# Kernel optimization log

Hardware: AMD Instinct MI355X
Metric: run time of the kernel (lower is better)

## Reference

```python
import jax, jax.numpy as jnp
import numpy as np
from jax import lax

H, W = 480, 640
EPS = 1e-20
DN = ('NCHW', 'OIHW', 'NCHW')


def _nconv(x, c, w_raw, b, pad):
    # Normalized convolution: positive weights via softplus (EnforcePos hook).
    w = jax.nn.softplus(w_raw)                     # (O, I, kh, kw)
    pads = [(pad, pad), (pad, pad)]
    denom = lax.conv_general_dilated(c, w, (1, 1), pads, dimension_numbers=DN)
    nomin = lax.conv_general_dilated(x * c, w, (1, 1), pads, dimension_numbers=DN)
    out = nomin / (denom + EPS) + b.reshape(1, -1, 1, 1)
    s = w.reshape(w.shape[0], -1).sum(-1).reshape(1, -1, 1, 1)  # per-out-ch weight sum
    return out, denom / s


def _pool2(x, c):
    # max_pool2d(c, 2, 2, return_indices=True) + gather of x at the argmax
    # locations (vectorized form of the per-(b,c) Python gather loops).
    B, C, h, w = c.shape
    cb = c.reshape(B, C, h // 2, 2, w // 2, 2).transpose(0, 1, 2, 4, 3, 5).reshape(B, C, h // 2, w // 2, 4)
    xb = x.reshape(B, C, h // 2, 2, w // 2, 2).transpose(0, 1, 2, 4, 3, 5).reshape(B, C, h // 2, w // 2, 4)
    idx = jnp.argmax(cb, axis=-1)
    c_ds = jnp.max(cb, axis=-1)
    x_ds = jnp.take_along_axis(xb, idx[..., None], axis=-1)[..., 0]
    return x_ds, c_ds


def _up2(a):
    return jnp.repeat(jnp.repeat(a, 2, axis=2), 2, axis=3)


def _adaptive_mat(n_in, n_out):
    # 1D adaptive average pooling as a (n_out, n_in) averaging matrix
    i = np.arange(n_out)
    st = (i * n_in) // n_out
    en = -((-(i + 1) * n_in) // n_out)  # ceil division
    M = np.zeros((n_out, n_in), np.float32)
    for r in range(n_out):
        M[r, st[r]:en[r]] = 1.0 / (en[r] - st[r])
    return jnp.asarray(M)


def _forward(S, w1, b1, w2, b2, w3, b3, w4, b4, w5, b5, w6, b6, w65, b65, w7, b7):
    c0 = (S > 0.01).astype(S.dtype)
    x1, c1 = _nconv(S, c0, w1, b1, 2)
    x1, c1 = _nconv(x1, c1, w2, b2, 2)
    x1, c1 = _nconv(x1, c1, w3, b3, 2)
    # scale 1/2
    x1_ds, c1_ds = _pool2(x1, c1)
    c1_ds = c1_ds / 4
    x2_ds, c2_ds = _nconv(x1_ds, c1_ds, w2, b2, 2)
    x2_ds, c2_ds = _nconv(x2_ds, c2_ds, w3, b3, 2)
    # scale 1/4
    x2_dss, c2_dss = _pool2(x2_ds, c2_ds)
    c2_dss = c2_dss / 4
    x3_ds, c3_ds = _nconv(x2_dss, c2_dss, w2, b2, 2)
    # scale 1/8
    x3_dss, c3_dss = _pool2(x3_ds, c3_ds)
    c3_dss = c3_dss / 4
    x4_ds, c4_ds = _nconv(x3_dss, c3_dss, w2, b2, 2)
    # decoder
    x4, c4 = _up2(x4_ds), _up2(c4_ds)
    x34_ds, c34_ds = _nconv(jnp.concatenate((x3_ds, x4), 1), jnp.concatenate((c3_ds, c4), 1), w4, b4, 1)
    x34, c34 = _up2(x34_ds), _up2(c34_ds)
    x23_ds, c23_ds = _nconv(jnp.concatenate((x2_ds, x34), 1), jnp.concatenate((c2_ds, c34), 1), w5, b5, 1)
    x23, c23 = _up2(x23_ds), _up2(c23_ds)
    xo, co = _nconv(jnp.concatenate((x23, x1), 1), jnp.concatenate((c23, c1), 1), w6, b6, 0)  # shrinks by 2
    xo, co = _nconv(xo, co, w65, b65, 1)
    xo, co = _nconv(xo, co, w7, b7, 0)
    Mh = _adaptive_mat(xo.shape[2], H)
    Mw = _adaptive_mat(xo.shape[3], W)
    return jnp.einsum('oi,bcij,pj->bcop', Mh, xo, Mw)


def setup_inputs() -> dict:
    key = jax.random.key(0)
    ks = jax.random.split(key, 20)
    B = 8
    d = {
        'fout': jax.random.normal(ks[0], (B, 3, H, W), jnp.float32),
        'S': jax.random.uniform(ks[1], (B, 1, H, W), jnp.float32),
        'K': jax.random.normal(ks[2], (B, 3, 3), jnp.float32),
    }
    shapes = {'w1': (4, 1, 5, 5), 'w2': (4, 4, 5, 5), 'w3': (4, 4, 5, 5),
              'w4': (4, 8, 3, 3), 'w5': (4, 8, 3, 3), 'w6': (4, 8, 3, 3),
              'w65': (4, 4, 3, 3), 'w7': (1, 4, 1, 1)}
    i = 3
    for name, sh in shapes.items():
        d[name] = 0.1 * jax.random.normal(ks[i], sh, jnp.float32)
        i += 1
        d['b' + name[1:]] = 0.01 * jax.random.normal(ks[i], (sh[0],), jnp.float32)
        i += 1
    return d


def reference(fout, S, K, w1, b1, w2, b2, w3, b3, w4, b4, w5, b5, w6, b6, w65, b65, w7, b7):
    # fout and K are accepted but unused by the original forward.
    return _forward(S, w1, b1, w2, b2, w3, b3, w4, b4, w5, b5, w6, b6, w65, b65, w7, b7)
```

## Files before the change

kernel.cpp:

```cpp
#include <hip/hip_runtime.h>


#define EPSN 1e-20f

typedef float v2f __attribute__((ext_vector_type(2)));

__device__ __forceinline__ float softplusf(float x) {
    return fmaxf(x, 0.f) + log1pf(expf(-fabsf(x)));
}
__device__ __forceinline__ float rcpf(float x) { return __builtin_amdgcn_rcpf(x); }

__device__ __forceinline__ void wsum4(const float4* s_w4, int n, int tid, float4* dst)
{
    if (tid < 64) {
        float4 a = make_float4(0.f, 0.f, 0.f, 0.f);
        for (int i = tid; i < n; i += 64) {
            float4 w = s_w4[i];
            a.x += w.x; a.y += w.y; a.z += w.z; a.w += w.w;
        }
        #pragma unroll
        for (int off = 32; off; off >>= 1) {
            a.x += __shfl_xor(a.x, off);
            a.y += __shfl_xor(a.y, off);
            a.z += __shfl_xor(a.z, off);
            a.w += __shfl_xor(a.w, off);
        }
        if (tid == 0) *dst = a;
    }
}

__device__ __forceinline__ void tap4(v2f v, v2f w01, v2f w23, v2f* a)
{
    asm("v_pk_fma_f32 %0, %1, %2, %0 op_sel:[0,0,0] op_sel_hi:[1,0,1]"
        : "+v"(a[0]) : "v"(w01), "v"(v));
    asm("v_pk_fma_f32 %0, %1, %2, %0 op_sel:[0,0,0] op_sel_hi:[1,0,1]"
        : "+v"(a[1]) : "v"(w23), "v"(v));
    asm("v_pk_fma_f32 %0, %1, %2, %0 op_sel:[0,1,0] op_sel_hi:[1,1,1]"
        : "+v"(a[2]) : "v"(w01), "v"(v));
    asm("v_pk_fma_f32 %0, %1, %2, %0 op_sel:[0,1,0] op_sel_hi:[1,1,1]"
        : "+v"(a[3]) : "v"(w23), "v"(v));
}
#define TAP2(W01, W23, VA, VB)  tap4((VA),(W01),(W23),aA); tap4((VB),(W01),(W23),aB);

#define NC_EPI(A, XO, CO)                                            \
    XO.x = A[2].x*rcpf(A[0].x+EPSN)+bias.x; CO.x = A[0].x*rs0;       \
    XO.y = A[2].y*rcpf(A[0].y+EPSN)+bias.y; CO.y = A[0].y*rs1;       \
    XO.z = A[3].x*rcpf(A[1].x+EPSN)+bias.z; CO.z = A[1].x*rs2;       \
    XO.w = A[3].y*rcpf(A[1].y+EPSN)+bias.w; CO.w = A[1].y*rs3;

#define NC_STORE_PACKED(HOUT, WOUT)                                         \
    {                                                                       \
        const int oh = oh0 + ty, ow = ow0 + 2 * tx;                         \
        if (oh < (HOUT) && ow < (WOUT)) {                                   \
            float4 bias = s_bias, ssum = s_sum;                             \
            float rs0=rcpf(ssum.x), rs1=rcpf(ssum.y),                       \
                  rs2=rcpf(ssum.z), rs3=rcpf(ssum.w);                       \
            size_t t = ((size_t)b * (HOUT) + oh) * (WOUT) + ow;             \
            float4 xo, co;                                                  \
            NC_EPI(aA, xo, co)                                              \
            xout4[t] = xo; cout4[t] = co;                                   \
            if (ow + 1 < (WOUT)) {                                          \
                NC_EPI(aB, xo, co)                                          \
                xout4[t+1] = xo; cout4[t+1] = co;                           \
            }                                                               \
        }                                                                   \
    }

#define STAGE_WRITE(SDE, SDO, LY, J, CA, XA, CB, XB)                 \
    SDE[0][LY][J] = (v2f){(CA).x, (XA).x * (CA).x};                  \
    SDE[1][LY][J] = (v2f){(CA).y, (XA).y * (CA).y};                  \
    SDE[2][LY][J] = (v2f){(CA).z, (XA).z * (CA).z};                  \
    SDE[3][LY][J] = (v2f){(CA).w, (XA).w * (CA).w};                  \
    SDO[0][LY][J] = (v2f){(CB).x, (XB).x * (CB).x};                  \
    SDO[1][LY][J] = (v2f){(CB).y, (XB).y * (CB).y};                  \
    SDO[2][LY][J] = (v2f){(CB).z, (XB).z * (CB).z};                  \
    SDO[3][LY][J] = (v2f){(CB).w, (XB).w * (CB).w};

__global__ __launch_bounds__(256) void nconv5_first(
    const float* __restrict__ S,
    const float* __restrict__ wraw, const float* __restrict__ braw,
    float4* __restrict__ xout4, float4* __restrict__ cout4,
    int Hh, int Ww)
{
    __shared__ v2f sdE[20][19], sdO[20][19];
    __shared__ float4 s_w4[25];
    __shared__ float4 s_sum, s_bias;
    const int b = blockIdx.z;
    const int oh0 = blockIdx.y * 16, ow0 = blockIdx.x * 32;
    const int tx = threadIdx.x, ty = threadIdx.y, tid = ty * 16 + tx;

    if (tid < 25) {
        float4 w;
        w.x = softplusf(wraw[tid]);      w.y = softplusf(wraw[25 + tid]);
        w.z = softplusf(wraw[50 + tid]); w.w = softplusf(wraw[75 + tid]);
        s_w4[tid] = w;
    }
    if (tid == 0) s_bias = make_float4(braw[0], braw[1], braw[2], braw[3]);
    __syncthreads();

    for (int i = tid; i < 20 * 18; i += 256) {
        int ly = i / 18, j = i - ly * 18;
        int ih = oh0 - 2 + ly, iw = ow0 - 2 + 2 * j;
        float s0 = 0.f, s1 = 0.f;
        if ((unsigned)ih < (unsigned)Hh && iw >= 0 && iw < Ww - 1) {
            float2 t = *(const float2*)&S[((size_t)b * Hh + ih) * Ww + iw];
            s0 = t.x; s1 = t.y;
        }
        float c0 = (s0 > 0.01f) ? 1.f : 0.f;
        float c1 = (s1 > 0.01f) ? 1.f : 0.f;
        sdE[ly][j] = (v2f){c0, s0 * c0};
        sdO[ly][j] = (v2f){c1, s1 * c1};
    }
    wsum4(s_w4, 25, tid, &s_sum);
    __syncthreads();

    v2f aA[4] = {}, aB[4] = {};
    #pragma unroll
    for (int kj = 0; kj < 5; ++kj) {
        const v2f* rE = &sdE[ty + kj][tx];
        const v2f* rO = &sdO[ty + kj][tx];
        v2f e0 = rE[0], o0 = rO[0], e1 = rE[1], o1 = rO[1], e2 = rE[2], o2 = rO[2];
        const v2f* wr = (const v2f*)&s_w4[kj * 5];
        TAP2(wr[0], wr[1], e0, o0)
        TAP2(wr[2], wr[3], o0, e1)
        TAP2(wr[4], wr[5], e1, o1)
        TAP2(wr[6], wr[7], o1, e2)
        TAP2(wr[8], wr[9], e2, o2)
    }
    NC_STORE_PACKED(Hh, Ww)
}

template<bool POOL>
__global__ __launch_bounds__(256) void nconv5p4(
    const float4* __restrict__ xin4, const float4* __restrict__ cin4,
    const float* __restrict__ wraw, const float* __restrict__ braw,
    float4* __restrict__ xout4, float4* __restrict__ cout4,
    float4* __restrict__ xo_p, float4* __restrict__ co_p,
    int Hh, int Ww)
{
    __shared__ v2f sdE[4][20][19], sdO[4][20][19];
    __shared__ float4 s_w4[100];
    __shared__ float4 s_sum, s_bias;
    const int b = blockIdx.z;
    const int oh0 = blockIdx.y * 16, ow0 = blockIdx.x * 32;
    const int tx = threadIdx.x, ty = threadIdx.y, tid = ty * 16 + tx;

    const float4 z = make_float4(0.f, 0.f, 0.f, 0.f);
    float4 cA0 = z, xA0 = z, cB0 = z, xB0 = z;
    float4 cA1 = z, xA1 = z, cB1 = z, xB1 = z;
    const bool t1ok = tid < 104;
    {
        int ly = tid / 18, j = tid - (tid / 18) * 18;
        int ih = oh0 - 2 + ly, iw = ow0 - 2 + 2 * j;
        if ((unsigned)ih < (unsigned)Hh) {
            size_t rb = ((size_t)b * Hh + ih) * Ww;
            if ((unsigned)iw < (unsigned)Ww)       { cA0 = cin4[rb + iw];     xA0 = xin4[rb + iw]; }
            if ((unsigned)(iw + 1) < (unsigned)Ww) { cB0 = cin4[rb + iw + 1]; xB0 = xin4[rb + iw + 1]; }
        }
    }
    if (t1ok) {
        int i = tid + 256;
        int ly = i / 18, j = i - ly * 18;
        int ih = oh0 - 2 + ly, iw = ow0 - 2 + 2 * j;
        if ((unsigned)ih < (unsigned)Hh) {
            size_t rb = ((size_t)b * Hh + ih) * Ww;
            if ((unsigned)iw < (unsigned)Ww)       { cA1 = cin4[rb + iw];     xA1 = xin4[rb + iw]; }
            if ((unsigned)(iw + 1) < (unsigned)Ww) { cB1 = cin4[rb + iw + 1]; xB1 = xin4[rb + iw + 1]; }
        }
    }

    if (tid < 100) {
        float4 w;
        w.x = softplusf(wraw[tid]);       w.y = softplusf(wraw[100 + tid]);
        w.z = softplusf(wraw[200 + tid]); w.w = softplusf(wraw[300 + tid]);
        s_w4[tid] = w;
    }
    if (tid == 0) s_bias = make_float4(braw[0], braw[1], braw[2], braw[3]);
    __syncthreads();

    {
        int ly = tid / 18, j = tid - (tid / 18) * 18;
        STAGE_WRITE(sdE, sdO, ly, j, cA0, xA0, cB0, xB0)
    }
    if (t1ok) {
        int i = tid + 256;
        int ly = i / 18, j = i - ly * 18;
        STAGE_WRITE(sdE, sdO, ly, j, cA1, xA1, cB1, xB1)
    }
    wsum4(s_w4, 100, tid, &s_sum);
    __syncthreads();

    v2f aA[4] = {}, aB[4] = {};
    #pragma unroll 1
    for (int ci = 0; ci < 4; ++ci) {
        #pragma unroll
        for (int kj = 0; kj < 5; ++kj) {
            const v2f* rE = &sdE[ci][ty + kj][tx];
            const v2f* rO = &sdO[ci][ty + kj][tx];
            v2f e0 = rE[0], o0 = rO[0], e1 = rE[1], o1 = rO[1], e2 = rE[2], o2 = rO[2];
            const v2f* wr = (const v2f*)&s_w4[ci * 25 + kj * 5];
            TAP2(wr[0], wr[1], e0, o0)
            TAP2(wr[2], wr[3], o0, e1)
            TAP2(wr[4], wr[5], e1, o1)
            TAP2(wr[6], wr[7], o1, e2)
            TAP2(wr[8], wr[9], e2, o2)
        }
    }

    const int oh = oh0 + ty, ow = ow0 + 2 * tx;
    float4 bias = s_bias, ssum = s_sum;
    float rs0 = rcpf(ssum.x), rs1 = rcpf(ssum.y),
          rs2 = rcpf(ssum.z), rs3 = rcpf(ssum.w);
    float4 xoA, coA, xoB, coB;
    NC_EPI(aA, xoA, coA)
    NC_EPI(aB, xoB, coB)
    const bool rowok = oh < Hh, colA = ow < Ww, colB = ow + 1 < Ww;
    if (rowok && colA) {
        size_t t = ((size_t)b * Hh + oh) * Ww + ow;
        xout4[t] = xoA; cout4[t] = coA;
        if (colB) { xout4[t + 1] = xoB; cout4[t + 1] = coB; }
    }
    if (POOL) {
        float4 cb = coA, xb = xoA;
        if (coB.x > cb.x) { cb.x = coB.x; xb.x = xoB.x; }
        if (coB.y > cb.y) { cb.y = coB.y; xb.y = xoB.y; }
        if (coB.z > cb.z) { cb.z = coB.z; xb.z = xoB.z; }
        if (coB.w > cb.w) { cb.w = coB.w; xb.w = xoB.w; }
        float4 cb2, xb2;
        cb2.x = __shfl_down(cb.x, 16); xb2.x = __shfl_down(xb.x, 16);
        cb2.y = __shfl_down(cb.y, 16); xb2.y = __shfl_down(xb.y, 16);
        cb2.z = __shfl_down(cb.z, 16); xb2.z = __shfl_down(xb.z, 16);
        cb2.w = __shfl_down(cb.w, 16); xb2.w = __shfl_down(xb.w, 16);
        if (!(ty & 1) && rowok && colA) {
            if (cb2.x > cb.x) { cb.x = cb2.x; xb.x = xb2.x; }
            if (cb2.y > cb.y) { cb.y = cb2.y; xb.y = xb2.y; }
            if (cb2.z > cb.z) { cb.z = cb2.z; xb.z = xb2.z; }
            if (cb2.w > cb.w) { cb.w = cb2.w; xb.w = xb2.w; }
            cb.x *= 0.25f; cb.y *= 0.25f; cb.z *= 0.25f; cb.w *= 0.25f;
            size_t tp = ((size_t)b * (Hh >> 1) + (oh >> 1)) * (Ww >> 1) + (ow >> 1);
            xo_p[tp] = xb; co_p[tp] = cb;
        }
    }
}

template<bool UP_FIRST, int PAD>
__global__ __launch_bounds__(256) void nconv3cat(
    const float4* __restrict__ xd4, const float4* __restrict__ cd4,
    const float4* __restrict__ xu4, const float4* __restrict__ cu4,
    const float* __restrict__ wraw, const float* __restrict__ braw,
    float4* __restrict__ xout4, float4* __restrict__ cout4,
    int Hin, int Win)
{
    __shared__ v2f sdE[4][18][18], sdO[4][18][18];
    __shared__ v2f sup[4][10][19];
    __shared__ float4 s_w4[72];
    __shared__ float4 s_sum, s_bias;

    const int Hout = Hin - 2 + 2 * PAD, Wout = Win - 2 + 2 * PAD;
    const int Hu = Hin / 2, Wu = Win / 2;
    const int b = blockIdx.z;
    const int oh0 = blockIdx.y * 16, ow0 = blockIdx.x * 32;
    const int tx = threadIdx.x, ty = threadIdx.y, tid = ty * 16 + tx;

    const float4 z = make_float4(0.f, 0.f, 0.f, 0.f);
    float4 cA0 = z, xA0 = z, cB0 = z, xB0 = z;
    float4 cA1 = z, xA1 = z, cB1 = z, xB1 = z;
    float4 cU = z, xU = z;
    const bool t1ok = tid < 50, upok = tid < 180;
    {
        int ly = tid / 17, j = tid - (tid / 17) * 17;
        int ih = oh0 - PAD + ly, iw = ow0 - PAD + 2 * j;
        if ((unsigned)ih < (unsigned)Hin) {
            size_t rb = ((size_t)b * Hin + ih) * Win;
            if ((unsigned)iw < (unsigned)Win)       { cA0 = cd4[rb + iw];     xA0 = xd4[rb + iw]; }
            if ((unsigned)(iw + 1) < (unsigned)Win) { cB0 = cd4[rb + iw + 1]; xB0 = xd4[rb + iw + 1]; }
        }
    }
    if (t1ok) {
        int i = tid + 256;
        int ly = i / 17, j = i - ly * 17;
        int ih = oh0 - PAD + ly, iw = ow0 - PAD + 2 * j;
        if ((unsigned)ih < (unsigned)Hin) {
            size_t rb = ((size_t)b * Hin + ih) * Win;
            if ((unsigned)iw < (unsigned)Win)       { cA1 = cd4[rb + iw];     xA1 = xd4[rb + iw]; }
            if ((unsigned)(iw + 1) < (unsigned)Win) { cB1 = cd4[rb + iw + 1]; xB1 = xd4[rb + iw + 1]; }
        }
    }
    const int ru0 = (oh0 - PAD) >> 1, cu0 = (ow0 - PAD) >> 1;
    if (upok) {
        int r = tid / 18, k = tid - (tid / 18) * 18;
        int ur = ru0 + r, uc = cu0 + k;
        if ((unsigned)ur < (unsigned)Hu && (unsigned)uc < (unsigned)Wu) {
            size_t t = ((size_t)b * Hu + ur) * Wu + uc;
            cU = cu4[t]; xU = xu4[t];
        }
    }

    if (tid < 72) {
        float4 w;
        w.x = softplusf(wraw[tid]);       w.y = softplusf(wraw[72 + tid]);
        w.z = softplusf(wraw[144 + tid]); w.w = softplusf(wraw[216 + tid]);
        s_w4[tid] = w;
    }
    if (tid == 0) s_bias = make_float4(braw[0], braw[1], braw[2], braw[3]);
    __syncthreads();

    {
        int ly = tid / 17, j = tid - (tid / 17) * 17;
        STAGE_WRITE(sdE, sdO, ly, j, cA0, xA0, cB0, xB0)
    }
    if (t1ok) {
        int i = tid + 256;
        int ly = i / 17, j = i - ly * 17;
        STAGE_WRITE(sdE, sdO, ly, j, cA1, xA1, cB1, xB1)
    }
    if (upok) {
        int r = tid / 18, k = tid - (tid / 18) * 18;
        sup[0][r][k] = (v2f){cU.x, xU.x * cU.x};
        sup[1][r][k] = (v2f){cU.y, xU.y * cU.y};
        sup[2][r][k] = (v2f){cU.z, xU.z * cU.z};
        sup[3][r][k] = (v2f){cU.w, xU.w * cU.w};
    }
    wsum4(s_w4, 72, tid, &s_sum);
    __syncthreads();

    v2f aA[4] = {}, aB[4] = {};
    #pragma unroll 1
    for (int ci = 0; ci < 4; ++ci) {
        const int chD = UP_FIRST ? ci + 4 : ci;
        const int chU = UP_FIRST ? ci : ci + 4;
        #pragma unroll
        for (int kj = 0; kj < 3; ++kj) {
            const v2f* rE = &sdE[ci][ty + kj][tx];
            const v2f* rO = &sdO[ci][ty + kj][tx];
            v2f e0 = rE[0], o0 = rO[0], e1 = rE[1], o1 = rO[1];
            const v2f* wr = (const v2f*)&s_w4[chD * 9 + kj * 3];
            TAP2(wr[0], wr[1], e0, o0)
            TAP2(wr[2], wr[3], o0, e1)
            TAP2(wr[4], wr[5], e1, o1)
        }
        #pragma unroll
        for (int kj = 0; kj < 3; ++kj) {
            int lyu = (ty + kj + PAD) >> 1;
            const v2f* ru = &sup[ci][lyu][tx];
            v2f u0 = ru[0], u1 = ru[1];
            v2f q0, q1, q2, q3;
            if (PAD == 1) {
                v2f u2 = ru[2];
                q0 = u0; q1 = u1; q2 = u1; q3 = u2;
            } else {
                q0 = u0; q1 = u0; q2 = u1; q3 = u1;
            }
            const v2f* wr = (const v2f*)&s_w4[chU * 9 + kj * 3];
            TAP2(wr[0], wr[1], q0, q1)
            TAP2(wr[2], wr[3], q1, q2)
            TAP2(wr[4], wr[5], q2, q3)
        }
    }
    NC_STORE_PACKED(Hout, Wout)
}

__global__ __launch_bounds__(256) void nconv3p_w7(
    const float4* __restrict__ xin4, const float4* __restrict__ cin4,
    const float* __restrict__ wraw, const float* __restrict__ braw,
    const float* __restrict__ w7raw, const float* __restrict__ b7raw,
    float* __restrict__ zout,
    int Hh, int Ww)
{
    __shared__ v2f sdE[4][18][18], sdO[4][18][18];
    __shared__ float4 s_w4[36];
    __shared__ float4 s_sum, s_bias, s_w7;
    __shared__ float s_b7;
    const int b = blockIdx.z;
    const int oh0 = blockIdx.y * 16, ow0 = blockIdx.x * 32;
    const int tx = threadIdx.x, ty = threadIdx.y, tid = ty * 16 + tx;

    const float4 z = make_float4(0.f, 0.f, 0.f, 0.f);
    float4 cA0 = z, xA0 = z, cB0 = z, xB0 = z;
    float4 cA1 = z, xA1 = z, cB1 = z, xB1 = z;
    const bool t1ok = tid < 50;
    {
        int ly = tid / 17, j = tid - (tid / 17) * 17;
        int ih = oh0 - 1 + ly, iw = ow0 - 1 + 2 * j;
        if ((unsigned)ih < (unsigned)Hh) {
            size_t rb = ((size_t)b * Hh + ih) * Ww;
            if ((unsigned)iw < (unsigned)Ww)       { cA0 = cin4[rb + iw];     xA0 = xin4[rb + iw]; }
            if ((unsigned)(iw + 1) < (unsigned)Ww) { cB0 = cin4[rb + iw + 1]; xB0 = xin4[rb + iw + 1]; }
        }
    }
    if (t1ok) {
        int i = tid + 256;
        int ly = i / 17, j = i - ly * 17;
        int ih = oh0 - 1 + ly, iw = ow0 - 1 + 2 * j;
        if ((unsigned)ih < (unsigned)Hh) {
            size_t rb = ((size_t)b * Hh + ih) * Ww;
            if ((unsigned)iw < (unsigned)Ww)       { cA1 = cin4[rb + iw];     xA1 = xin4[rb + iw]; }
            if ((unsigned)(iw + 1) < (unsigned)Ww) { cB1 = cin4[rb + iw + 1]; xB1 = xin4[rb + iw + 1]; }
        }
    }

    if (tid < 36) {
        float4 w;
        w.x = softplusf(wraw[tid]);      w.y = softplusf(wraw[36 + tid]);
        w.z = softplusf(wraw[72 + tid]); w.w = softplusf(wraw[108 + tid]);
        s_w4[tid] = w;
    }
    if (tid == 0) {
        s_bias = make_float4(braw[0], braw[1], braw[2], braw[3]);
        s_w7 = make_float4(softplusf(w7raw[0]), softplusf(w7raw[1]),
                           softplusf(w7raw[2]), softplusf(w7raw[3]));
        s_b7 = b7raw[0];
    }
    __syncthreads();

    {
        int ly = tid / 17, j = tid - (tid / 17) * 17;
        STAGE_WRITE(sdE, sdO, ly, j, cA0, xA0, cB0, xB0)
    }
    if (t1ok) {
        int i = tid + 256;
        int ly = i / 17, j = i - ly * 17;
        STAGE_WRITE(sdE, sdO, ly, j, cA1, xA1, cB1, xB1)
    }
    wsum4(s_w4, 36, tid, &s_sum);
    __syncthreads();

    v2f aA[4] = {}, aB[4] = {};
    #pragma unroll 1
    for (int ci = 0; ci < 4; ++ci) {
        #pragma unroll
        for (int kj = 0; kj < 3; ++kj) {
            const v2f* rE = &sdE[ci][ty + kj][tx];
            const v2f* rO = &sdO[ci][ty + kj][tx];
            v2f e0 = rE[0], o0 = rO[0], e1 = rE[1], o1 = rO[1];
            const v2f* wr = (const v2f*)&s_w4[ci * 9 + kj * 3];
            TAP2(wr[0], wr[1], e0, o0)
            TAP2(wr[2], wr[3], o0, e1)
            TAP2(wr[4], wr[5], e1, o1)
        }
    }

    const int oh = oh0 + ty, ow = ow0 + 2 * tx;
    if (oh >= Hh || ow >= Ww) return;
    float4 bias = s_bias, ssum = s_sum, w7 = s_w7;
    float b7 = s_b7;
    float rs0 = rcpf(ssum.x), rs1 = rcpf(ssum.y),
          rs2 = rcpf(ssum.z), rs3 = rcpf(ssum.w);
    float4 xo, co;
    NC_EPI(aA, xo, co)
    float den7 = w7.x * co.x + w7.y * co.y + w7.z * co.z + w7.w * co.w;
    float nom7 = w7.x * xo.x * co.x + w7.y * xo.y * co.y
               + w7.z * xo.z * co.z + w7.w * xo.w * co.w;
    float zA = nom7 * rcpf(den7 + EPSN) + b7;
    size_t t = ((size_t)b * Hh + oh) * Ww + ow;
    if (ow + 1 < Ww) {
        NC_EPI(aB, xo, co)
        den7 = w7.x * co.x + w7.y * co.y + w7.z * co.z + w7.w * co.w;
        nom7 = w7.x * xo.x * co.x + w7.y * xo.y * co.y
             + w7.z * xo.z * co.z + w7.w * xo.w * co.w;
        float zB = nom7 * rcpf(den7 + EPSN) + b7;
        *(float2*)&zout[t] = make_float2(zA, zB);
    } else {
        zout[t] = zA;
    }
}

__global__ __launch_bounds__(256) void apoolk(
    const float* __restrict__ in, float* __restrict__ out)
{
    const int HI = 478, WI = 638, HO = 480, WO = 640;
    int total = 8 * HO * WO;
    int i = blockIdx.x * 256 + threadIdx.x;
    if (i >= total) return;
    int ow = i % WO;
    int oh = (i / WO) % HO;
    int b  = i / (WO * HO);
    int sh = (oh * HI) / HO, eh = ((oh + 1) * HI + HO - 1) / HO;
    int sw = (ow * WI) / WO, ew = ((ow + 1) * WI + WO - 1) / WO;
    float s = 0.f;
    for (int ih = sh; ih < eh; ++ih)
        for (int iw = sw; iw < ew; ++iw)
            s += in[((size_t)b * HI + ih) * WI + iw];
    out[i] = s * rcpf((float)((eh - sh) * (ew - sw)));
}

extern "C" void kernel_launch(void* const* d_in, const int* in_sizes, int n_in,
                              void* d_out, int out_size, void* d_ws, size_t ws_size,
                              hipStream_t stream)
{
    const float* S   = (const float*)d_in[1];
    const float* w1  = (const float*)d_in[3];  const float* b1  = (const float*)d_in[4];
    const float* w2  = (const float*)d_in[5];  const float* b2  = (const float*)d_in[6];
    const float* w3  = (const float*)d_in[7];  const float* b3  = (const float*)d_in[8];
    const float* w4  = (const float*)d_in[9];  const float* b4  = (const float*)d_in[10];
    const float* w5  = (const float*)d_in[11]; const float* b5  = (const float*)d_in[12];
    const float* w6  = (const float*)d_in[13]; const float* b6  = (const float*)d_in[14];
    const float* w65 = (const float*)d_in[15]; const float* b65 = (const float*)d_in[16];
    const float* w7  = (const float*)d_in[17]; const float* b7  = (const float*)d_in[18];
    float* out = (float*)d_out;
    float* ws  = (float*)d_ws;

    const size_t FULL = 9830400, HALF = 2457600, QUAR = 614400, EIGH = 153600;
    float4 *A0 = (float4*)ws,              *A1 = (float4*)(ws + FULL),
           *A2 = (float4*)(ws + 2*FULL),   *A3 = (float4*)(ws + 3*FULL);
    float4 *P0 = (float4*)(ws + 4*FULL),            *P1 = (float4*)(ws + 4*FULL + HALF),
           *P2 = (float4*)(ws + 4*FULL + 2*HALF),   *P3 = (float4*)(ws + 4*FULL + 3*HALF);
    float4 *Q0 = (float4*)(ws + 4*FULL + 4*HALF),          *Q1 = (float4*)(ws + 4*FULL + 4*HALF + QUAR),
           *Q2 = (float4*)(ws + 4*FULL + 4*HALF + 2*QUAR), *Q3 = (float4*)(ws + 4*FULL + 4*HALF + 3*QUAR);
    float4 *E0 = (float4*)(ws + 4*FULL + 4*HALF + 4*QUAR),
           *E1 = (float4*)(ws + 4*FULL + 4*HALF + 4*QUAR + EIGH),
           *E2 = (float4*)(ws + 4*FULL + 4*HALF + 4*QUAR + 2*EIGH),
           *E3 = (float4*)(ws + 4*FULL + 4*HALF + 4*QUAR + 3*EIGH);

    dim3 blk(16, 16);
    auto grd = [](int Ho, int Wo) { return dim3((Wo + 31) / 32, (Ho + 15) / 16, 8); };

    nconv5_first<<<grd(480, 640), blk, 0, stream>>>(S, w1, b1, A0, A1, 480, 640);
    nconv5p4<false><<<grd(480, 640), blk, 0, stream>>>(A0, A1, w2, b2, A2, A3, nullptr, nullptr, 480, 640);
    nconv5p4<true ><<<grd(480, 640), blk, 0, stream>>>(A2, A3, w3, b3, A0, A1, P0, P1, 480, 640);
    nconv5p4<false><<<grd(240, 320), blk, 0, stream>>>(P0, P1, w2, b2, P2, P3, nullptr, nullptr, 240, 320);
    nconv5p4<true ><<<grd(240, 320), blk, 0, stream>>>(P2, P3, w3, b3, P0, P1, Q0, Q1, 240, 320);
    nconv5p4<true ><<<grd(120, 160), blk, 0, stream>>>(Q0, Q1, w2, b2, Q2, Q3, E0, E1, 120, 160);
    nconv5p4<false><<<grd(60, 80), blk, 0, stream>>>(E0, E1, w2, b2, E2, E3, nullptr, nullptr, 60, 80);
    nconv3cat<false, 1><<<grd(120, 160), blk, 0, stream>>>(Q2, Q3, E2, E3, w4, b4, Q0, Q1, 120, 160);
    nconv3cat<false, 1><<<grd(240, 320), blk, 0, stream>>>(P0, P1, Q0, Q1, w5, b5, P2, P3, 240, 320);
    nconv3cat<true , 0><<<grd(478, 638), blk, 0, stream>>>(A0, A1, P2, P3, w6, b6, A2, A3, 480, 640);
    nconv3p_w7<<<grd(478, 638), blk, 0, stream>>>(A2, A3, w65, b65, w7, b7, (float*)A0, 478, 638);
    apoolk<<<(8 * 480 * 640 + 255) / 256, 256, 0, stream>>>((float*)A0, out);
}
```

Before: 342.3 us.

## Precompute softplus weights once and feed taps from scalar registers

Adds a one-block prep kernel that applies softplus to every layer's weights, computes the per-channel weight sums and packs them with the biases into a small buffer at the start of the output. Each conv kernel then reads its weights straight from that uniform global buffer instead of recomputing softplus, reducing, and staging weights in LDS per block, which removes one barrier and redundant transcendental work. The packed FMA inline asm now takes the weights as SGPR operands, so weight loads can become scalar loads and VGPR pressure drops. The risks are an extra launch, and the scratch buffer in d_out is safe only because apoolk overwrites it last.

```diff
diff --git a/kernel.cpp b/kernel.cpp
--- a/kernel.cpp
+++ b/kernel.cpp
@@ -10,37 +10,20 @@
 }
 __device__ __forceinline__ float rcpf(float x) { return __builtin_amdgcn_rcpf(x); }
 
-__device__ __forceinline__ void wsum4(const float4* s_w4, int n, int tid, float4* dst)
-{
-    if (tid < 64) {
-        float4 a = make_float4(0.f, 0.f, 0.f, 0.f);
-        for (int i = tid; i < n; i += 64) {
-            float4 w = s_w4[i];
-            a.x += w.x; a.y += w.y; a.z += w.z; a.w += w.w;
-        }
-        #pragma unroll
-        for (int off = 32; off; off >>= 1) {
-            a.x += __shfl_xor(a.x, off);
-            a.y += __shfl_xor(a.y, off);
-            a.z += __shfl_xor(a.z, off);
-            a.w += __shfl_xor(a.w, off);
-        }
-        if (tid == 0) *dst = a;
-    }
-}
-
 __device__ __forceinline__ void tap4(v2f v, v2f w01, v2f w23, v2f* a)
 {
     asm("v_pk_fma_f32 %0, %1, %2, %0 op_sel:[0,0,0] op_sel_hi:[1,0,1]"
-        : "+v"(a[0]) : "v"(w01), "v"(v));
+        : "+v"(a[0]) : "s"(w01), "v"(v));
     asm("v_pk_fma_f32 %0, %1, %2, %0 op_sel:[0,0,0] op_sel_hi:[1,0,1]"
-        : "+v"(a[1]) : "v"(w23), "v"(v));
+        : "+v"(a[1]) : "s"(w23), "v"(v));
     asm("v_pk_fma_f32 %0, %1, %2, %0 op_sel:[0,1,0] op_sel_hi:[1,1,1]"
-        : "+v"(a[2]) : "v"(w01), "v"(v));
+        : "+v"(a[2]) : "s"(w01), "v"(v));
     asm("v_pk_fma_f32 %0, %1, %2, %0 op_sel:[0,1,0] op_sel_hi:[1,1,1]"
-        : "+v"(a[3]) : "v"(w23), "v"(v));
-}
-#define TAP2(W01, W23, VA, VB)  tap4((VA),(W01),(W23),aA); tap4((VB),(W01),(W23),aB);
+        : "+v"(a[3]) : "s"(w23), "v"(v));
+}
+#define TAPW(W, VA, VB)                                                     \
+    { v2f w01_ = {(W).x, (W).y}, w23_ = {(W).z, (W).w};                     \
+      tap4((VA), w01_, w23_, aA); tap4((VB), w01_, w23_, aB); }
 
 #define NC_EPI(A, XO, CO)                                            \
     XO.x = A[2].x*rcpf(A[0].x+EPSN)+bias.x; CO.x = A[0].x*rs0;       \
@@ -52,7 +35,7 @@
     {                                                                       \
         const int oh = oh0 + ty, ow = ow0 + 2 * tx;                         \
         if (oh < (HOUT) && ow < (WOUT)) {                                   \
-            float4 bias = s_bias, ssum = s_sum;                             \
+            float4 bias = g_bias, ssum = g_sum;                             \
             float rs0=rcpf(ssum.x), rs1=rcpf(ssum.y),                       \
                   rs2=rcpf(ssum.z), rs3=rcpf(ssum.w);                       \
             size_t t = ((size_t)b * (HOUT) + oh) * (WOUT) + ow;             \
@@ -76,27 +59,75 @@
     SDO[2][LY][J] = (v2f){(CB).z, (XB).z * (CB).z};                  \
     SDO[3][LY][J] = (v2f){(CB).w, (XB).w * (CB).w};
 
+
+__global__ __launch_bounds__(256) void prepw(
+    const float* __restrict__ w1, const float* __restrict__ b1,
+    const float* __restrict__ w2, const float* __restrict__ b2,
+    const float* __restrict__ w3, const float* __restrict__ b3,
+    const float* __restrict__ w4, const float* __restrict__ b4,
+    const float* __restrict__ w5, const float* __restrict__ b5,
+    const float* __restrict__ w6, const float* __restrict__ b6,
+    const float* __restrict__ w65, const float* __restrict__ b65,
+    const float* __restrict__ w7, const float* __restrict__ b7,
+    float4* __restrict__ WP)
+{
+    const int tid = threadIdx.x;
+    if (tid < 25)  WP[0 + tid]   = make_float4(softplusf(w1[tid]),  softplusf(w1[25 + tid]),
+                                               softplusf(w1[50 + tid]), softplusf(w1[75 + tid]));
+    if (tid < 100) WP[27 + tid]  = make_float4(softplusf(w2[tid]),  softplusf(w2[100 + tid]),
+                                               softplusf(w2[200 + tid]), softplusf(w2[300 + tid]));
+    if (tid < 100) WP[129 + tid] = make_float4(softplusf(w3[tid]),  softplusf(w3[100 + tid]),
+                                               softplusf(w3[200 + tid]), softplusf(w3[300 + tid]));
+    if (tid < 72)  WP[231 + tid] = make_float4(softplusf(w4[tid]),  softplusf(w4[72 + tid]),
+                                               softplusf(w4[144 + tid]), softplusf(w4[216 + tid]));
+    if (tid < 72)  WP[305 + tid] = make_float4(softplusf(w5[tid]),  softplusf(w5[72 + tid]),
+                                               softplusf(w5[144 + tid]), softplusf(w5[216 + tid]));
+    if (tid < 72)  WP[379 + tid] = make_float4(softplusf(w6[tid]),  softplusf(w6[72 + tid]),
+                                               softplusf(w6[144 + tid]), softplusf(w6[216 + tid]));
+    if (tid < 36)  WP[453 + tid] = make_float4(softplusf(w65[tid]), softplusf(w65[36 + tid]),
+                                               softplusf(w65[72 + tid]), softplusf(w65[108 + tid]));
+    if (tid == 0) {
+        WP[26]  = make_float4(b1[0], b1[1], b1[2], b1[3]);
+        WP[128] = make_float4(b2[0], b2[1], b2[2], b2[3]);
+        WP[230] = make_float4(b3[0], b3[1], b3[2], b3[3]);
+        WP[304] = make_float4(b4[0], b4[1], b4[2], b4[3]);
+        WP[378] = make_float4(b5[0], b5[1], b5[2], b5[3]);
+        WP[452] = make_float4(b6[0], b6[1], b6[2], b6[3]);
+        WP[490] = make_float4(b65[0], b65[1], b65[2], b65[3]);
+        WP[491] = make_float4(softplusf(w7[0]), softplusf(w7[1]),
+                              softplusf(w7[2]), softplusf(w7[3]));
+        WP[492] = make_float4(b7[0], 0.f, 0.f, 0.f);
+    }
+    __syncthreads();
+    int base = -1, cnt = 0;
+    if      (tid == 0) { base = 0;   cnt = 25;  }
+    else if (tid == 1) { base = 27;  cnt = 100; }
+    else if (tid == 2) { base = 129; cnt = 100; }
+    else if (tid == 3) { base = 231; cnt = 72;  }
+    else if (tid == 4) { base = 305; cnt = 72;  }
+    else if (tid == 5) { base = 379; cnt = 72;  }
+    else if (tid == 6) { base = 453; cnt = 36;  }
+    if (base >= 0) {
+        float4 s = make_float4(0.f, 0.f, 0.f, 0.f);
+        for (int i = 0; i < cnt; ++i) {
+            float4 w = WP[base + i];
+            s.x += w.x; s.y += w.y; s.z += w.z; s.w += w.w;
+        }
+        WP[base + cnt] = s;
+    }
+}
+
 __global__ __launch_bounds__(256) void nconv5_first(
-    const float* __restrict__ S,
-    const float* __restrict__ wraw, const float* __restrict__ braw,
+    const float* __restrict__ S, const float4* __restrict__ WP,
     float4* __restrict__ xout4, float4* __restrict__ cout4,
     int Hh, int Ww)
 {
     __shared__ v2f sdE[20][19], sdO[20][19];
-    __shared__ float4 s_w4[25];
-    __shared__ float4 s_sum, s_bias;
     const int b = blockIdx.z;
     const int oh0 = blockIdx.y * 16, ow0 = blockIdx.x * 32;
     const int tx = threadIdx.x, ty = threadIdx.y, tid = ty * 16 + tx;
 
-    if (tid < 25) {
-        float4 w;
-        w.x = softplusf(wraw[tid]);      w.y = softplusf(wraw[25 + tid]);
-        w.z = softplusf(wraw[50 + tid]); w.w = softplusf(wraw[75 + tid]);
-        s_w4[tid] = w;
-    }
-    if (tid == 0) s_bias = make_float4(braw[0], braw[1], braw[2], braw[3]);
-    __syncthreads();
+    const float4 g_sum = WP[25], g_bias = WP[26];
 
     for (int i = tid; i < 20 * 18; i += 256) {
         int ly = i / 18, j = i - ly * 18;
@@ -111,7 +142,6 @@
         sdE[ly][j] = (v2f){c0, s0 * c0};
         sdO[ly][j] = (v2f){c1, s1 * c1};
     }
-    wsum4(s_w4, 25, tid, &s_sum);
     __syncthreads();
 
     v2f aA[4] = {}, aB[4] = {};
@@ -120,12 +150,13 @@
         const v2f* rE = &sdE[ty + kj][tx];
         const v2f* rO = &sdO[ty + kj][tx];
         v2f e0 = rE[0], o0 = rO[0], e1 = rE[1], o1 = rO[1], e2 = rE[2], o2 = rO[2];
-        const v2f* wr = (const v2f*)&s_w4[kj * 5];
-        TAP2(wr[0], wr[1], e0, o0)
-        TAP2(wr[2], wr[3], o0, e1)
-        TAP2(wr[4], wr[5], e1, o1)
-        TAP2(wr[6], wr[7], o1, e2)
-        TAP2(wr[8], wr[9], e2, o2)
+        const float4* wp = WP + kj * 5;
+        float4 W0 = wp[0], W1 = wp[1], W2 = wp[2], W3 = wp[3], W4 = wp[4];
+        TAPW(W0, e0, o0)
+        TAPW(W1, o0, e1)
+        TAPW(W2, e1, o1)
+        TAPW(W3, o1, e2)
+        TAPW(W4, e2, o2)
     }
     NC_STORE_PACKED(Hh, Ww)
 }
@@ -133,17 +164,17 @@
 template<bool POOL>
 __global__ __launch_bounds__(256) void nconv5p4(
     const float4* __restrict__ xin4, const float4* __restrict__ cin4,
-    const float* __restrict__ wraw, const float* __restrict__ braw,
+    const float4* __restrict__ WP, int wb,
     float4* __restrict__ xout4, float4* __restrict__ cout4,
     float4* __restrict__ xo_p, float4* __restrict__ co_p,
     int Hh, int Ww)
 {
     __shared__ v2f sdE[4][20][19], sdO[4][20][19];
-    __shared__ float4 s_w4[100];
-    __shared__ float4 s_sum, s_bias;
     const int b = blockIdx.z;
     const int oh0 = blockIdx.y * 16, ow0 = blockIdx.x * 32;
     const int tx = threadIdx.x, ty = threadIdx.y, tid = ty * 16 + tx;
+
+    const float4 g_sum = WP[wb + 100], g_bias = WP[wb + 101];
 
     const float4 z = make_float4(0.f, 0.f, 0.f, 0.f);
     float4 cA0 = z, xA0 = z, cB0 = z, xB0 = z;
@@ -168,16 +199,6 @@
             if ((unsigned)(iw + 1) < (unsigned)Ww) { cB1 = cin4[rb + iw + 1]; xB1 = xin4[rb + iw + 1]; }
         }
     }
-
-    if (tid < 100) {
-        float4 w;
-        w.x = softplusf(wraw[tid]);       w.y = softplusf(wraw[100 + tid]);
-        w.z = softplusf(wraw[200 + tid]); w.w = softplusf(wraw[300 + tid]);
-        s_w4[tid] = w;
-    }
-    if (tid == 0) s_bias = make_float4(braw[0], braw[1], braw[2], braw[3]);
-    __syncthreads();
-
     {
         int ly = tid / 18, j = tid - (tid / 18) * 18;
         STAGE_WRITE(sdE, sdO, ly, j, cA0, xA0, cB0, xB0)
@@ -187,28 +208,29 @@
         int ly = i / 18, j = i - ly * 18;
         STAGE_WRITE(sdE, sdO, ly, j, cA1, xA1, cB1, xB1)
     }
-    wsum4(s_w4, 100, tid, &s_sum);
     __syncthreads();
 
     v2f aA[4] = {}, aB[4] = {};
     #pragma unroll 1
     for (int ci = 0; ci < 4; ++ci) {
+        const float4* wp = WP + wb + ci * 25;
         #pragma unroll
         for (int kj = 0; kj < 5; ++kj) {
             const v2f* rE = &sdE[ci][ty + kj][tx];
             const v2f* rO = &sdO[ci][ty + kj][tx];
             v2f e0 = rE[0], o0 = rO[0], e1 = rE[1], o1 = rO[1], e2 = rE[2], o2 = rO[2];
-            const v2f* wr = (const v2f*)&s_w4[ci * 25 + kj * 5];
-            TAP2(wr[0], wr[1], e0, o0)
-            TAP2(wr[2], wr[3], o0, e1)
-            TAP2(wr[4], wr[5], e1, o1)
-            TAP2(wr[6], wr[7], o1, e2)
-            TAP2(wr[8], wr[9], e2, o2)
+            float4 W0 = wp[kj * 5], W1 = wp[kj * 5 + 1], W2 = wp[kj * 5 + 2],
+                   W3 = wp[kj * 5 + 3], W4 = wp[kj * 5 + 4];
+            TAPW(W0, e0, o0)
+            TAPW(W1, o0, e1)
+            TAPW(W2, e1, o1)
+            TAPW(W3, o1, e2)
+            TAPW(W4, e2, o2)
         }
     }
 
     const int oh = oh0 + ty, ow = ow0 + 2 * tx;
-    float4 bias = s_bias, ssum = s_sum;
+    float4 bias = g_bias, ssum = g_sum;
     float rs0 = rcpf(ssum.x), rs1 = rcpf(ssum.y),
           rs2 = rcpf(ssum.z), rs3 = rcpf(ssum.w);
     float4 xoA, coA, xoB, coB;
@@ -247,20 +269,19 @@
 __global__ __launch_bounds__(256) void nconv3cat(
     const float4* __restrict__ xd4, const float4* __restrict__ cd4,
     const float4* __restrict__ xu4, const float4* __restrict__ cu4,
-    const float* __restrict__ wraw, const float* __restrict__ braw,
+    const float4* __restrict__ WP, int wb,
     float4* __restrict__ xout4, float4* __restrict__ cout4,
     int Hin, int Win)
 {
     __shared__ v2f sdE[4][18][18], sdO[4][18][18];
     __shared__ v2f sup[4][10][19];
-    __shared__ float4 s_w4[72];
-    __shared__ float4 s_sum, s_bias;
-
     const int Hout = Hin - 2 + 2 * PAD, Wout = Win - 2 + 2 * PAD;
     const int Hu = Hin / 2, Wu = Win / 2;
     const int b = blockIdx.z;
     const int oh0 = blockIdx.y * 16, ow0 = blockIdx.x * 32;
     const int tx = threadIdx.x, ty = threadIdx.y, tid = ty * 16 + tx;
+
+    const float4 g_sum = WP[wb + 72], g_bias = WP[wb + 73];
 
     const float4 z = make_float4(0.f, 0.f, 0.f, 0.f);
     float4 cA0 = z, xA0 = z, cB0 = z, xB0 = z;
@@ -295,16 +316,6 @@
             cU = cu4[t]; xU = xu4[t];
         }
     }
-
-    if (tid < 72) {
-        float4 w;
-        w.x = softplusf(wraw[tid]);       w.y = softplusf(wraw[72 + tid]);
-        w.z = softplusf(wraw[144 + tid]); w.w = softplusf(wraw[216 + tid]);
-        s_w4[tid] = w;
-    }
-    if (tid == 0) s_bias = make_float4(braw[0], braw[1], braw[2], braw[3]);
-    __syncthreads();
-
     {
         int ly = tid / 17, j = tid - (tid / 17) * 17;
         STAGE_WRITE(sdE, sdO, ly, j, cA0, xA0, cB0, xB0)
@@ -321,7 +332,6 @@
         sup[2][r][k] = (v2f){cU.z, xU.z * cU.z};
         sup[3][r][k] = (v2f){cU.w, xU.w * cU.w};
     }
-    wsum4(s_w4, 72, tid, &s_sum);
     __syncthreads();
 
     v2f aA[4] = {}, aB[4] = {};
@@ -334,10 +344,11 @@
             const v2f* rE = &sdE[ci][ty + kj][tx];
             const v2f* rO = &sdO[ci][ty + kj][tx];
             v2f e0 = rE[0], o0 = rO[0], e1 = rE[1], o1 = rO[1];
-            const v2f* wr = (const v2f*)&s_w4[chD * 9 + kj * 3];
-            TAP2(wr[0], wr[1], e0, o0)
-            TAP2(wr[2], wr[3], o0, e1)
-            TAP2(wr[4], wr[5], e1, o1)
+            const float4* wp = WP + wb + chD * 9 + kj * 3;
+            float4 W0 = wp[0], W1 = wp[1], W2 = wp[2];
+            TAPW(W0, e0, o0)
+            TAPW(W1, o0, e1)
+            TAPW(W2, e1, o1)
         }
         #pragma unroll
         for (int kj = 0; kj < 3; ++kj) {
@@ -351,10 +362,11 @@
             } else {
                 q0 = u0; q1 = u0; q2 = u1; q3 = u1;
             }
-            const v2f* wr = (const v2f*)&s_w4[chU * 9 + kj * 3];
-            TAP2(wr[0], wr[1], q0, q1)
-            TAP2(wr[2], wr[3], q1, q2)
-            TAP2(wr[4], wr[5], q2, q3)
+            const float4* wp = WP + wb + chU * 9 + kj * 3;
+            float4 W0 = wp[0], W1 = wp[1], W2 = wp[2];
+            TAPW(W0, q0, q1)
+            TAPW(W1, q1, q2)
+            TAPW(W2, q2, q3)
         }
     }
     NC_STORE_PACKED(Hout, Wout)
@@ -362,18 +374,18 @@
 
 __global__ __launch_bounds__(256) void nconv3p_w7(
     const float4* __restrict__ xin4, const float4* __restrict__ cin4,
-    const float* __restrict__ wraw, const float* __restrict__ braw,
-    const float* __restrict__ w7raw, const float* __restrict__ b7raw,
+    const float4* __restrict__ WP,
     float* __restrict__ zout,
     int Hh, int Ww)
 {
     __shared__ v2f sdE[4][18][18], sdO[4][18][18];
-    __shared__ float4 s_w4[36];
-    __shared__ float4 s_sum, s_bias, s_w7;
-    __shared__ float s_b7;
     const int b = blockIdx.z;
     const int oh0 = blockIdx.y * 16, ow0 = blockIdx.x * 32;
     const int tx = threadIdx.x, ty = threadIdx.y, tid = ty * 16 + tx;
+
+    const float4 g_sum = WP[489], g_bias = WP[490];
+    const float4 w7 = WP[491];
+    const float b7 = WP[492].x;
 
     const float4 z = make_float4(0.f, 0.f, 0.f, 0.f);
     float4 cA0 = z, xA0 = z, cB0 = z, xB0 = z;
@@ -398,21 +410,6 @@
             if ((unsigned)(iw + 1) < (unsigned)Ww) { cB1 = cin4[rb + iw + 1]; xB1 = xin4[rb + iw + 1]; }
         }
     }
-
-    if (tid < 36) {
-        float4 w;
-        w.x = softplusf(wraw[tid]);      w.y = softplusf(wraw[36 + tid]);
-        w.z = softplusf(wraw[72 + tid]); w.w = softplusf(wraw[108 + tid]);
-        s_w4[tid] = w;
-    }
-    if (tid == 0) {
-        s_bias = make_float4(braw[0], braw[1], braw[2], braw[3]);
-        s_w7 = make_float4(softplusf(w7raw[0]), softplusf(w7raw[1]),
-                           softplusf(w7raw[2]), softplusf(w7raw[3]));
-        s_b7 = b7raw[0];
-    }
-    __syncthreads();
-
     {
         int ly = tid / 17, j = tid - (tid / 17) * 17;
         STAGE_WRITE(sdE, sdO, ly, j, cA0, xA0, cB0, xB0)
@@ -422,28 +419,27 @@
         int ly = i / 17, j = i - ly * 17;
         STAGE_WRITE(sdE, sdO, ly, j, cA1, xA1, cB1, xB1)
     }
-    wsum4(s_w4, 36, tid, &s_sum);
     __syncthreads();
 
     v2f aA[4] = {}, aB[4] = {};
     #pragma unroll 1
     for (int ci = 0; ci < 4; ++ci) {
+        const float4* wp = WP + 453 + ci * 9;
         #pragma unroll
         for (int kj = 0; kj < 3; ++kj) {
             const v2f* rE = &sdE[ci][ty + kj][tx];
             const v2f* rO = &sdO[ci][ty + kj][tx];
             v2f e0 = rE[0], o0 = rO[0], e1 = rE[1], o1 = rO[1];
-            const v2f* wr = (const v2f*)&s_w4[ci * 9 + kj * 3];
-            TAP2(wr[0], wr[1], e0, o0)
-            TAP2(wr[2], wr[3], o0, e1)
-            TAP2(wr[4], wr[5], e1, o1)
+            float4 W0 = wp[kj * 3], W1 = wp[kj * 3 + 1], W2 = wp[kj * 3 + 2];
+            TAPW(W0, e0, o0)
+            TAPW(W1, o0, e1)
+            TAPW(W2, e1, o1)
         }
     }
 
     const int oh = oh0 + ty, ow = ow0 + 2 * tx;
     if (oh >= Hh || ow >= Ww) return;
-    float4 bias = s_bias, ssum = s_sum, w7 = s_w7;
-    float b7 = s_b7;
+    float4 bias = g_bias, ssum = g_sum;
     float rs0 = rcpf(ssum.x), rs1 = rcpf(ssum.y),
           rs2 = rcpf(ssum.z), rs3 = rcpf(ssum.w);
     float4 xo, co;
@@ -512,19 +508,24 @@
            *E2 = (float4*)(ws + 4*FULL + 4*HALF + 4*QUAR + 2*EIGH),
            *E3 = (float4*)(ws + 4*FULL + 4*HALF + 4*QUAR + 3*EIGH);
 
+    float4* WP = (float4*)d_out;
+
     dim3 blk(16, 16);
     auto grd = [](int Ho, int Wo) { return dim3((Wo + 31) / 32, (Ho + 15) / 16, 8); };
 
-    nconv5_first<<<grd(480, 640), blk, 0, stream>>>(S, w1, b1, A0, A1, 480, 640);
-    nconv5p4<false><<<grd(480, 640), blk, 0, stream>>>(A0, A1, w2, b2, A2, A3, nullptr, nullptr, 480, 640);
-    nconv5p4<true ><<<grd(480, 640), blk, 0, stream>>>(A2, A3, w3, b3, A0, A1, P0, P1, 480, 640);
-    nconv5p4<false><<<grd(240, 320), blk, 0, stream>>>(P0, P1, w2, b2, P2, P3, nullptr, nullptr, 240, 320);
-    nconv5p4<true ><<<grd(240, 320), blk, 0, stream>>>(P2, P3, w3, b3, P0, P1, Q0, Q1, 240, 320);
-    nconv5p4<true ><<<grd(120, 160), blk, 0, stream>>>(Q0, Q1, w2, b2, Q2, Q3, E0, E1, 120, 160);
-    nconv5p4<false><<<grd(60, 80), blk, 0, stream>>>(E0, E1, w2, b2, E2, E3, nullptr, nullptr, 60, 80);
-    nconv3cat<false, 1><<<grd(120, 160), blk, 0, stream>>>(Q2, Q3, E2, E3, w4, b4, Q0, Q1, 120, 160);
-    nconv3cat<false, 1><<<grd(240, 320), blk, 0, stream>>>(P0, P1, Q0, Q1, w5, b5, P2, P3, 240, 320);
-    nconv3cat<true , 0><<<grd(478, 638), blk, 0, stream>>>(A0, A1, P2, P3, w6, b6, A2, A3, 480, 640);
-    nconv3p_w7<<<grd(478, 638), blk, 0, stream>>>(A2, A3, w65, b65, w7, b7, (float*)A0, 478, 638);
+    prepw<<<1, 256, 0, stream>>>(w1, b1, w2, b2, w3, b3, w4, b4, w5, b5,
+                                 w6, b6, w65, b65, w7, b7, WP);
+
+    nconv5_first<<<grd(480, 640), blk, 0, stream>>>(S, WP, A0, A1, 480, 640);
+    nconv5p4<false><<<grd(480, 640), blk, 0, stream>>>(A0, A1, WP, 27, A2, A3, nullptr, nullptr, 480, 640);
+    nconv5p4<true ><<<grd(480, 640), blk, 0, stream>>>(A2, A3, WP, 129, A0, A1, P0, P1, 480, 640);
+    nconv5p4<false><<<grd(240, 320), blk, 0, stream>>>(P0, P1, WP, 27, P2, P3, nullptr, nullptr, 240, 320);
+    nconv5p4<true ><<<grd(240, 320), blk, 0, stream>>>(P2, P3, WP, 129, P0, P1, Q0, Q1, 240, 320);
+    nconv5p4<true ><<<grd(120, 160), blk, 0, stream>>>(Q0, Q1, WP, 27, Q2, Q3, E0, E1, 120, 160);
+    nconv5p4<false><<<grd(60, 80), blk, 0, stream>>>(E0, E1, WP, 27, E2, E3, nullptr, nullptr, 60, 80);
+    nconv3cat<false, 1><<<grd(120, 160), blk, 0, stream>>>(Q2, Q3, E2, E3, WP, 231, Q0, Q1, 120, 160);
+    nconv3cat<false, 1><<<grd(240, 320), blk, 0, stream>>>(P0, P1, Q0, Q1, WP, 305, P2, P3, 240, 320);
+    nconv3cat<true , 0><<<grd(478, 638), blk, 0, stream>>>(A0, A1, P2, P3, WP, 379, A2, A3, 480, 640);
+    nconv3p_w7<<<grd(478, 638), blk, 0, stream>>>(A2, A3, WP, (float*)A0, 478, 638);
     apoolk<<<(8 * 480 * 640 + 255) / 256, 256, 0, stream>>>((float*)A0, out);
 }
```

After: 299.5 us, median of 2. 1.14x faster.
